# Performance work log

Hardware: AMD Instinct MI355X
Metric: run time of the kernel (lower is better)

The kernel has to match this reference:

```python
import jax, jax.numpy as jnp
import numpy as np

N_HEAD = 16
NEG = -1e9

def setup_inputs() -> dict:
    key = jax.random.key(0)
    k1, k2, k3 = jax.random.split(key, 3)
    B, S, NX = 8, 1024, 1024
    x = jax.random.normal(k1, (B, S, NX), dtype=jnp.float32)
    w_attn = jax.random.normal(k2, (NX, 3 * NX), dtype=jnp.float32) * 0.02
    b_attn = jnp.zeros((3 * NX,), dtype=jnp.float32)
    w_proj = jax.random.normal(k3, (NX, NX), dtype=jnp.float32) * 0.02
    b_proj = jnp.zeros((NX,), dtype=jnp.float32)
    return {"x": x, "w_attn": w_attn, "b_attn": b_attn, "w_proj": w_proj, "b_proj": b_proj}

def reference(x, w_attn, b_attn, w_proj, b_proj):
    B, S, NX = x.shape
    H = N_HEAD
    D = NX // H
    qkv = x @ w_attn + b_attn                      # [B,S,3*NX]
    q, k, v = jnp.split(qkv, 3, axis=-1)           # each [B,S,NX]
    q = q.reshape(B, S, H, D)
    k = k.reshape(B, S, H, D)
    v = v.reshape(B, S, H, D)
    # scores with scale (scale=True -> divide by sqrt(head_dim))
    w = jnp.einsum('bqhd,bkhd->bhqk', q, k) / jnp.sqrt(jnp.float32(D))
    tril = jnp.tril(jnp.ones((S, S), dtype=w.dtype))  # causal mask buffer
    w = w * tril + NEG * (1.0 - tril)
    w = jax.nn.softmax(w, axis=-1)                 # dropout is identity at eval
    a = jnp.einsum('bhqk,bkhd->bqhd', w, v)        # [B,S,H,D]
    a = a.reshape(B, S, NX)
    a = a @ w_proj + b_proj
    return a
```

## Files before the change

kernel.cpp:

```cpp
#include <hip/hip_runtime.h>
#include <hip/hip_bf16.h>
#include <stdint.h>

typedef __bf16 bf16x8 __attribute__((ext_vector_type(8)));
typedef float  f32x4  __attribute__((ext_vector_type(4)));
typedef float  f32x16 __attribute__((ext_vector_type(16)));

__device__ __forceinline__ void gload_lds16(const void* g, void* l) {
  __builtin_amdgcn_global_load_lds(
      (const __attribute__((address_space(1))) unsigned int*)g,
      (__attribute__((address_space(3))) unsigned int*)l, 16, 0, 0);
}

__global__ void k_cast(const float* __restrict__ in, __bf16* __restrict__ out, int n4) {
  int i = blockIdx.x * blockDim.x + threadIdx.x;
  if (i >= n4) return;
  float4 v = reinterpret_cast<const float4*>(in)[i];
  union { __bf16 h[4]; uint64_t u; } c;
  c.h[0] = (__bf16)v.x; c.h[1] = (__bf16)v.y; c.h[2] = (__bf16)v.z; c.h[3] = (__bf16)v.w;
  *reinterpret_cast<uint64_t*>(out + 4l * i) = c.u;
}

__global__ void k_transpose_cast(const float* __restrict__ in, __bf16* __restrict__ out,
                                 int R, int C) {
  __shared__ float t[32][33];
  const int tx = threadIdx.x & 31, ty = threadIdx.x >> 5;
  const int c0 = blockIdx.x * 32, r0 = blockIdx.y * 32;
#pragma unroll
  for (int rr = 0; rr < 4; ++rr)
    t[ty * 4 + rr][tx] = in[(long)(r0 + ty * 4 + rr) * C + c0 + tx];
  __syncthreads();
#pragma unroll
  for (int rr = 0; rr < 4; ++rr)
    out[(long)(c0 + ty * 4 + rr) * R + r0 + tx] = (__bf16)t[tx][ty * 4 + rr];
}

template <int MODE>
__global__ void k_gemm_bt(const __bf16* __restrict__ A, const __bf16* __restrict__ Bt,
                          const float* __restrict__ bias, int M, int N, int K,
                          __bf16* __restrict__ qo, __bf16* __restrict__ ko,
                          __bf16* __restrict__ vo, float* __restrict__ fo) {
  __shared__ __bf16 Ab[128 * 32];
  __shared__ __bf16 Bb[128 * 32];
  const int l = threadIdx.x & 63, w = threadIdx.x >> 6;
  const int wr = w >> 1, wc = w & 1;
  const int bm = blockIdx.y, bn = blockIdx.x;

  f32x4 acc[4][4] = {};

  const __bf16* Ag = A + (long)(bm * 128 + w * 32 + (l >> 2)) * K + (l & 3) * 8;
  const __bf16* Bg = Bt + (long)(bn * 128 + w * 32 + (l >> 2)) * K + (l & 3) * 8;
  char* Al = (char*)Ab + w * 2048;
  char* Bl = (char*)Bb + w * 2048;

  for (int k0 = 0; k0 < K; k0 += 32) {
    gload_lds16(Ag + k0, Al);
    gload_lds16(Ag + 16l * K + k0, Al + 1024);
    gload_lds16(Bg + k0, Bl);
    gload_lds16(Bg + 16l * K + k0, Bl + 1024);
    __syncthreads();

    bf16x8 af[4], bfr[4];
#pragma unroll
    for (int mi = 0; mi < 4; ++mi)
      af[mi] = *(const bf16x8*)&Ab[(wr * 64 + mi * 16 + (l & 15)) * 32 + ((l >> 4) << 3)];
#pragma unroll
    for (int ni = 0; ni < 4; ++ni)
      bfr[ni] = *(const bf16x8*)&Bb[(wc * 64 + ni * 16 + (l & 15)) * 32 + ((l >> 4) << 3)];
#pragma unroll
    for (int mi = 0; mi < 4; ++mi)
#pragma unroll
      for (int ni = 0; ni < 4; ++ni)
        acc[mi][ni] = __builtin_amdgcn_mfma_f32_16x16x32_bf16(af[mi], bfr[ni], acc[mi][ni], 0, 0, 0);
    __syncthreads();
  }

  if (MODE == 0) {
#pragma unroll
    for (int ni = 0; ni < 4; ++ni) {
      const int c = bn * 128 + wc * 64 + ni * 16 + (l & 15);
      const float bv = bias[c];
      const int which = c >> 10, cc = c & 1023, h = cc >> 6, d = cc & 63;
#pragma unroll
      for (int mi = 0; mi < 4; ++mi)
#pragma unroll
        for (int i = 0; i < 4; ++i) {
          const int r = bm * 128 + wr * 64 + mi * 16 + ((l >> 4) << 2) + i;
          const int b = r >> 10, s_ = r & 1023;
          float fv = acc[mi][ni][i] + bv;
          if (which == 0) fv *= 0.125f;
          const __bf16 v = (__bf16)fv;
          const long hb = (long)(b * 16 + h);
          if (which == 0)      qo[(hb * 1024 + s_) * 64 + d] = v;
          else if (which == 1) ko[(hb * 1024 + s_) * 64 + d] = v;
          else                 vo[(hb * 64 + d) * 1024 + s_] = v;
        }
    }
  } else {
#pragma unroll
    for (int ni = 0; ni < 4; ++ni) {
      const int c = bn * 128 + wc * 64 + ni * 16 + (l & 15);
      const float bv = bias[c];
#pragma unroll
      for (int mi = 0; mi < 4; ++mi)
#pragma unroll
        for (int i = 0; i < 4; ++i) {
          const int r = bm * 128 + wr * 64 + mi * 16 + ((l >> 4) << 2) + i;
          fo[(long)r * N + c] = acc[mi][ni][i] + bv;
        }
    }
  }
}

__device__ __forceinline__ void attn_qtile(const __bf16* __restrict__ Q,
                                           const __bf16* __restrict__ Kh,
                                           const __bf16* __restrict__ Vt,
                                           __bf16* __restrict__ ob,
                                           int b, int h, int qbw, int l) {
  const int lm = l & 31, hi = l >> 5;

  bf16x8 qf[4];
#pragma unroll
  for (int ds = 0; ds < 4; ++ds)
    qf[ds] = *(const bf16x8*)(Q + (long)(qbw + lm) * 64 + ds * 16 + hi * 8);

  f32x16 oacc0 = {}, oacc1 = {};
  float m = -__builtin_inff(), s = 0.f;

  const int ntiles = (qbw >> 5) + 1;
  for (int kt = 0; kt < ntiles; ++kt) {
    const int k0 = kt * 32;
    f32x16 st = {};
#pragma unroll
    for (int ds = 0; ds < 4; ++ds) {
      bf16x8 kf = *(const bf16x8*)(Kh + (long)(k0 + lm) * 64 + ds * 16 + hi * 8);
      st = __builtin_amdgcn_mfma_f32_32x32x16_bf16(kf, qf[ds], st, 0, 0, 0);
    }
    if (kt == ntiles - 1) {
      const int q = qbw + lm;
#pragma unroll
      for (int r = 0; r < 16; ++r) {
        const int key = k0 + (r & 3) + 8 * (r >> 2) + 4 * hi;
        if (key > q) st[r] = -__builtin_inff();
      }
    }
    float tm = st[0];
#pragma unroll
    for (int r = 1; r < 16; ++r) tm = fmaxf(tm, st[r]);
    tm = fmaxf(tm, __shfl_xor(tm, 32));
    if (!__all(tm <= m + 8.f)) {
      const float mn = fmaxf(m, tm);
      const float fac = __expf(m - mn);
      m = mn;
      s *= fac;
#pragma unroll
      for (int r = 0; r < 16; ++r) {
        const int qr = (r & 3) + 8 * (r >> 2) + 4 * hi;
        const float fr = __int_as_float(
            __builtin_amdgcn_ds_bpermute(qr * 4, __float_as_int(fac)));
        oacc0[r] *= fr; oacc1[r] *= fr;
      }
    }
    float p[16], ts = 0.f;
#pragma unroll
    for (int r = 0; r < 16; ++r) { p[r] = __expf(st[r] - m); ts += p[r]; }
    ts += __shfl_xor(ts, 32);
    s += ts;
    unsigned int w8[8];
#pragma unroll
    for (int t = 0; t < 8; ++t) {
      union { __bf16 hh[2]; unsigned int u; } pk;
      pk.hh[0] = (__bf16)p[2 * t]; pk.hh[1] = (__bf16)p[2 * t + 1];
      w8[t] = pk.u;
    }
    const unsigned int e0 = __shfl_xor(hi ? w8[0] : w8[2], 32);
    const unsigned int e1 = __shfl_xor(hi ? w8[1] : w8[3], 32);
    const unsigned int e2 = __shfl_xor(hi ? w8[4] : w8[6], 32);
    const unsigned int e3 = __shfl_xor(hi ? w8[5] : w8[7], 32);
    union { unsigned int wd[4]; bf16x8 v; } pa0, pa1;
    if (hi) {
      pa0.wd[0] = e0;    pa0.wd[1] = e1;    pa0.wd[2] = w8[2]; pa0.wd[3] = w8[3];
      pa1.wd[0] = e2;    pa1.wd[1] = e3;    pa1.wd[2] = w8[6]; pa1.wd[3] = w8[7];
    } else {
      pa0.wd[0] = w8[0]; pa0.wd[1] = w8[1]; pa0.wd[2] = e0;    pa0.wd[3] = e1;
      pa1.wd[0] = w8[4]; pa1.wd[1] = w8[5]; pa1.wd[2] = e2;    pa1.wd[3] = e3;
    }
#pragma unroll
    for (int t = 0; t < 2; ++t) {
      const bf16x8 pa = t ? pa1.v : pa0.v;
      bf16x8 vf0 = *(const bf16x8*)(Vt + (long)lm * 1024 + k0 + t * 16 + hi * 8);
      bf16x8 vf1 = *(const bf16x8*)(Vt + (long)(32 + lm) * 1024 + k0 + t * 16 + hi * 8);
      oacc0 = __builtin_amdgcn_mfma_f32_32x32x16_bf16(pa, vf0, oacc0, 0, 0, 0);
      oacc1 = __builtin_amdgcn_mfma_f32_32x32x16_bf16(pa, vf1, oacc1, 0, 0, 0);
    }
  }
  const float invs = 1.f / s;
#pragma unroll
  for (int r = 0; r < 16; ++r) {
    const int qr = (r & 3) + 8 * (r >> 2) + 4 * hi;
    const float inv = __int_as_float(
        __builtin_amdgcn_ds_bpermute(qr * 4, __float_as_int(invs)));
    const long row = (long)(b * 1024 + qbw + qr) * 1024 + h * 64;
    ob[row + lm]      = (__bf16)(oacc0[r] * inv);
    ob[row + 32 + lm] = (__bf16)(oacc1[r] * inv);
  }
}

__global__ void k_attn(const __bf16* __restrict__ qb_, const __bf16* __restrict__ kb,
                       const __bf16* __restrict__ vtb, __bf16* __restrict__ ob) {
  const int l = threadIdx.x & 63, w = threadIdx.x >> 6;
  const int bh = blockIdx.y, b = bh >> 4, h = bh & 15;
  const int wi = blockIdx.x * 4 + w;
  const __bf16* Q  = qb_ + (long)bh * 65536;
  const __bf16* Kh = kb  + (long)bh * 65536;
  const __bf16* Vt = vtb + (long)bh * 65536;
  attn_qtile(Q, Kh, Vt, ob, b, h, wi * 32, l);
  attn_qtile(Q, Kh, Vt, ob, b, h, (31 - wi) * 32, l);
}

extern "C" void kernel_launch(void* const* d_in, const int* in_sizes, int n_in,
                              void* d_out, int out_size, void* d_ws, size_t ws_size,
                              hipStream_t stream) {
  const float* x      = (const float*)d_in[0];
  const float* w_attn = (const float*)d_in[1];
  const float* b_attn = (const float*)d_in[2];
  const float* w_proj = (const float*)d_in[3];
  const float* b_proj = (const float*)d_in[4];
  float* out = (float*)d_out;

  char* ws = (char*)d_ws;
  const size_t SZ_XBF = (size_t)8192 * 1024 * 2;
  __bf16* x_bf = (__bf16*)ws;  ws += SZ_XBF;
  __bf16* wat  = (__bf16*)ws;  ws += (size_t)3072 * 1024 * 2;
  __bf16* wpt  = (__bf16*)ws;  ws += (size_t)1024 * 1024 * 2;
  __bf16* qb   = (__bf16*)ws;  ws += SZ_XBF;
  __bf16* kb   = (__bf16*)ws;  ws += SZ_XBF;
  __bf16* vtb  = (__bf16*)ws;  ws += SZ_XBF;
  __bf16* obf  = (__bf16*)ws;  ws += SZ_XBF;

  k_cast<<<8192, 256, 0, stream>>>(x, x_bf, 2097152);
  k_transpose_cast<<<dim3(96, 32), 256, 0, stream>>>(w_attn, wat, 1024, 3072);
  k_transpose_cast<<<dim3(32, 32), 256, 0, stream>>>(w_proj, wpt, 1024, 1024);
  k_gemm_bt<0><<<dim3(24, 64), 256, 0, stream>>>(x_bf, wat, b_attn, 8192, 3072, 1024,
                                                 qb, kb, vtb, nullptr);
  k_attn<<<dim3(4, 128), 256, 0, stream>>>(qb, kb, vtb, obf);
  k_gemm_bt<1><<<dim3(8, 64), 256, 0, stream>>>(obf, wpt, b_proj, 8192, 1024, 1024,
                                                nullptr, nullptr, nullptr, out);
}
```

Measured before the change: 286.9 us.

## Double-buffer swizzled GEMM, widen attention key tiles, add XCD-aware block mapping

The GEMM is rewritten with a 64-wide K step, a double-buffered LDS pipeline that uses explicit vmcnt waits, an XOR swizzle to avoid LDS bank conflicts, and MFMA priority boosting. Both GEMM and attention now map blocks so that neighbouring tiles or heads share an XCD for L2 reuse. The attention loop handles 64 keys per iteration instead of 32, which halves the number of softmax rescale and reduction steps. The trade-off is higher register pressure in attention and more LDS per block in the GEMM, which may lower occupancy.

```diff
diff --git a/kernel.cpp b/kernel.cpp
--- a/kernel.cpp
+++ b/kernel.cpp
@@ -5,6 +5,11 @@
 typedef __bf16 bf16x8 __attribute__((ext_vector_type(8)));
 typedef float  f32x4  __attribute__((ext_vector_type(4)));
 typedef float  f32x16 __attribute__((ext_vector_type(16)));
+
+#define BARRIER() asm volatile("s_barrier" ::: "memory")
+#define VMCNT(n)  asm volatile("s_waitcnt vmcnt(" #n ")" ::: "memory")
+#define LGKM0()   asm volatile("s_waitcnt lgkmcnt(0)" ::: "memory")
+#define SCHED0()  __builtin_amdgcn_sched_barrier(0)
 
 __device__ __forceinline__ void gload_lds16(const void* g, void* l) {
   __builtin_amdgcn_global_load_lds(
@@ -36,61 +41,98 @@
 }
 
 template <int MODE>
-__global__ void k_gemm_bt(const __bf16* __restrict__ A, const __bf16* __restrict__ Bt,
-                          const float* __restrict__ bias, int M, int N, int K,
-                          __bf16* __restrict__ qo, __bf16* __restrict__ ko,
-                          __bf16* __restrict__ vo, float* __restrict__ fo) {
-  __shared__ __bf16 Ab[128 * 32];
-  __shared__ __bf16 Bb[128 * 32];
-  const int l = threadIdx.x & 63, w = threadIdx.x >> 6;
-  const int wr = w >> 1, wc = w & 1;
-  const int bm = blockIdx.y, bn = blockIdx.x;
+__launch_bounds__(256, 2)
+__global__ void k_gemm2(const __bf16* __restrict__ A, const __bf16* __restrict__ Bt,
+                        const float* __restrict__ bias, int M, int N, int K, int NBX,
+                        __bf16* __restrict__ qo, __bf16* __restrict__ ko,
+                        __bf16* __restrict__ vo, float* __restrict__ fo) {
+  __shared__ __bf16 lds[2][2][8192];
+  const int tid = threadIdx.x;
+  const int l = tid & 63, w = tid >> 6;
+  const int lm = l & 15, lq = l >> 4;
+  const int wm = w >> 1, wn = w & 1;
+  const int xcd = blockIdx.x & 7, s = blockIdx.x >> 3;
+  const int bn = xcd * NBX + s % NBX;
+  const int bm = s / NBX;
+  const int nt = K >> 6;
+
+  const int rA = tid >> 3;
+  const int scol = (((tid & 7) * 16) ^ ((rA & 7) << 4)) >> 1;
+  long a_off[4], b_off[4];
+#pragma unroll
+  for (int li = 0; li < 4; ++li) {
+    a_off[li] = (long)(bm * 128 + li * 32 + rA) * K + scol;
+    b_off[li] = (long)(bn * 128 + li * 32 + rA) * K + scol;
+  }
+#define STAGE(buf, t) { \
+    gload_lds16(A + a_off[0] + (long)(t) * 64, &lds[buf][0][tid * 8]); \
+    gload_lds16(A + a_off[1] + (long)(t) * 64, &lds[buf][0][2048 + tid * 8]); \
+    gload_lds16(A + a_off[2] + (long)(t) * 64, &lds[buf][0][4096 + tid * 8]); \
+    gload_lds16(A + a_off[3] + (long)(t) * 64, &lds[buf][0][6144 + tid * 8]); \
+    gload_lds16(Bt + b_off[0] + (long)(t) * 64, &lds[buf][1][tid * 8]); \
+    gload_lds16(Bt + b_off[1] + (long)(t) * 64, &lds[buf][1][2048 + tid * 8]); \
+    gload_lds16(Bt + b_off[2] + (long)(t) * 64, &lds[buf][1][4096 + tid * 8]); \
+    gload_lds16(Bt + b_off[3] + (long)(t) * 64, &lds[buf][1][6144 + tid * 8]); }
+
+  const int aswz = (lm & 7) << 4;
+  const int cofs0 = ((0 * 64 + lq * 16) ^ aswz) >> 1;
+  const int cofs1 = ((1 * 64 + lq * 16) ^ aswz) >> 1;
+  const int arow = wm * 64 + lm;
+  const int brow = wn * 64 + lm;
 
   f32x4 acc[4][4] = {};
 
-  const __bf16* Ag = A + (long)(bm * 128 + w * 32 + (l >> 2)) * K + (l & 3) * 8;
-  const __bf16* Bg = Bt + (long)(bn * 128 + w * 32 + (l >> 2)) * K + (l & 3) * 8;
-  char* Al = (char*)Ab + w * 2048;
-  char* Bl = (char*)Bb + w * 2048;
-
-  for (int k0 = 0; k0 < K; k0 += 32) {
-    gload_lds16(Ag + k0, Al);
-    gload_lds16(Ag + 16l * K + k0, Al + 1024);
-    gload_lds16(Bg + k0, Bl);
-    gload_lds16(Bg + 16l * K + k0, Bl + 1024);
-    __syncthreads();
-
-    bf16x8 af[4], bfr[4];
-#pragma unroll
-    for (int mi = 0; mi < 4; ++mi)
-      af[mi] = *(const bf16x8*)&Ab[(wr * 64 + mi * 16 + (l & 15)) * 32 + ((l >> 4) << 3)];
-#pragma unroll
-    for (int ni = 0; ni < 4; ++ni)
-      bfr[ni] = *(const bf16x8*)&Bb[(wc * 64 + ni * 16 + (l & 15)) * 32 + ((l >> 4) << 3)];
-#pragma unroll
-    for (int mi = 0; mi < 4; ++mi)
-#pragma unroll
-      for (int ni = 0; ni < 4; ++ni)
-        acc[mi][ni] = __builtin_amdgcn_mfma_f32_16x16x32_bf16(af[mi], bfr[ni], acc[mi][ni], 0, 0, 0);
-    __syncthreads();
+  STAGE(0, 0);
+
+  for (int t = 0; t < nt; ++t) {
+    const int cur = t & 1;
+    if (t + 1 < nt) { STAGE(cur ^ 1, t + 1); VMCNT(8); }
+    else VMCNT(0);
+    BARRIER();
+    const __bf16* La = lds[cur][0];
+    const __bf16* Lbv = lds[cur][1];
+    bf16x8 af[4][2], bfr[4][2];
+#pragma unroll
+    for (int mi = 0; mi < 4; ++mi) {
+      af[mi][0] = *(const bf16x8*)&La[(arow + mi * 16) * 64 + cofs0];
+      af[mi][1] = *(const bf16x8*)&La[(arow + mi * 16) * 64 + cofs1];
+    }
+#pragma unroll
+    for (int ni = 0; ni < 4; ++ni) {
+      bfr[ni][0] = *(const bf16x8*)&Lbv[(brow + ni * 16) * 64 + cofs0];
+      bfr[ni][1] = *(const bf16x8*)&Lbv[(brow + ni * 16) * 64 + cofs1];
+    }
+    LGKM0(); SCHED0();
+    __builtin_amdgcn_s_setprio(1);
+#pragma unroll
+    for (int ks = 0; ks < 2; ++ks)
+#pragma unroll
+      for (int mi = 0; mi < 4; ++mi)
+#pragma unroll
+        for (int ni = 0; ni < 4; ++ni)
+          acc[mi][ni] = __builtin_amdgcn_mfma_f32_16x16x32_bf16(af[mi][ks], bfr[ni][ks],
+                                                                acc[mi][ni], 0, 0, 0);
+    __builtin_amdgcn_s_setprio(0);
+    SCHED0();
+    BARRIER();
   }
 
   if (MODE == 0) {
 #pragma unroll
     for (int ni = 0; ni < 4; ++ni) {
-      const int c = bn * 128 + wc * 64 + ni * 16 + (l & 15);
+      const int c = bn * 128 + wn * 64 + ni * 16 + lm;
       const float bv = bias[c];
-      const int which = c >> 10, cc = c & 1023, h = cc >> 6, d = cc & 63;
+      const int which = c >> 10, cc = c & 1023, hh = cc >> 6, d = cc & 63;
 #pragma unroll
       for (int mi = 0; mi < 4; ++mi)
 #pragma unroll
         for (int i = 0; i < 4; ++i) {
-          const int r = bm * 128 + wr * 64 + mi * 16 + ((l >> 4) << 2) + i;
+          const int r = bm * 128 + wm * 64 + mi * 16 + lq * 4 + i;
           const int b = r >> 10, s_ = r & 1023;
           float fv = acc[mi][ni][i] + bv;
           if (which == 0) fv *= 0.125f;
           const __bf16 v = (__bf16)fv;
-          const long hb = (long)(b * 16 + h);
+          const long hb = (long)(b * 16 + hh);
           if (which == 0)      qo[(hb * 1024 + s_) * 64 + d] = v;
           else if (which == 1) ko[(hb * 1024 + s_) * 64 + d] = v;
           else                 vo[(hb * 64 + d) * 1024 + s_] = v;
@@ -99,17 +141,18 @@
   } else {
 #pragma unroll
     for (int ni = 0; ni < 4; ++ni) {
-      const int c = bn * 128 + wc * 64 + ni * 16 + (l & 15);
+      const int c = bn * 128 + wn * 64 + ni * 16 + lm;
       const float bv = bias[c];
 #pragma unroll
       for (int mi = 0; mi < 4; ++mi)
 #pragma unroll
         for (int i = 0; i < 4; ++i) {
-          const int r = bm * 128 + wr * 64 + mi * 16 + ((l >> 4) << 2) + i;
+          const int r = bm * 128 + wm * 64 + mi * 16 + lq * 4 + i;
           fo[(long)r * N + c] = acc[mi][ni][i] + bv;
         }
     }
   }
+#undef STAGE
 }
 
 __device__ __forceinline__ void attn_qtile(const __bf16* __restrict__ Q,
@@ -127,26 +170,29 @@
   f32x16 oacc0 = {}, oacc1 = {};
   float m = -__builtin_inff(), s = 0.f;
 
-  const int ntiles = (qbw >> 5) + 1;
-  for (int kt = 0; kt < ntiles; ++kt) {
-    const int k0 = kt * 32;
-    f32x16 st = {};
+  const int nt64 = (qbw >> 6) + 1;
+  for (int kt = 0; kt < nt64; ++kt) {
+    const int k0 = kt * 64;
+    f32x16 st0 = {}, st1 = {};
 #pragma unroll
     for (int ds = 0; ds < 4; ++ds) {
-      bf16x8 kf = *(const bf16x8*)(Kh + (long)(k0 + lm) * 64 + ds * 16 + hi * 8);
-      st = __builtin_amdgcn_mfma_f32_32x32x16_bf16(kf, qf[ds], st, 0, 0, 0);
-    }
-    if (kt == ntiles - 1) {
+      bf16x8 kf0 = *(const bf16x8*)(Kh + (long)(k0 + lm) * 64 + ds * 16 + hi * 8);
+      bf16x8 kf1 = *(const bf16x8*)(Kh + (long)(k0 + 32 + lm) * 64 + ds * 16 + hi * 8);
+      st0 = __builtin_amdgcn_mfma_f32_32x32x16_bf16(kf0, qf[ds], st0, 0, 0, 0);
+      st1 = __builtin_amdgcn_mfma_f32_32x32x16_bf16(kf1, qf[ds], st1, 0, 0, 0);
+    }
+    if (kt == nt64 - 1) {
       const int q = qbw + lm;
 #pragma unroll
       for (int r = 0; r < 16; ++r) {
         const int key = k0 + (r & 3) + 8 * (r >> 2) + 4 * hi;
-        if (key > q) st[r] = -__builtin_inff();
+        if (key > q)      st0[r] = -__builtin_inff();
+        if (key + 32 > q) st1[r] = -__builtin_inff();
       }
     }
-    float tm = st[0];
-#pragma unroll
-    for (int r = 1; r < 16; ++r) tm = fmaxf(tm, st[r]);
+    float tm = fmaxf(st0[0], st1[0]);
+#pragma unroll
+    for (int r = 1; r < 16; ++r) tm = fmaxf(tm, fmaxf(st0[r], st1[r]));
     tm = fmaxf(tm, __shfl_xor(tm, 32));
     if (!__all(tm <= m + 8.f)) {
       const float mn = fmaxf(m, tm);
@@ -161,37 +207,59 @@
         oacc0[r] *= fr; oacc1[r] *= fr;
       }
     }
-    float p[16], ts = 0.f;
-#pragma unroll
-    for (int r = 0; r < 16; ++r) { p[r] = __expf(st[r] - m); ts += p[r]; }
+    float ts = 0.f;
+    unsigned int w8a[8], w8b[8];
+#pragma unroll
+    for (int t = 0; t < 8; ++t) {
+      const float pa_ = __expf(st0[2 * t] - m), pb_ = __expf(st0[2 * t + 1] - m);
+      ts += pa_ + pb_;
+      union { __bf16 hh[2]; unsigned int u; } pk;
+      pk.hh[0] = (__bf16)pa_; pk.hh[1] = (__bf16)pb_;
+      w8a[t] = pk.u;
+    }
+#pragma unroll
+    for (int t = 0; t < 8; ++t) {
+      const float pa_ = __expf(st1[2 * t] - m), pb_ = __expf(st1[2 * t + 1] - m);
+      ts += pa_ + pb_;
+      union { __bf16 hh[2]; unsigned int u; } pk;
+      pk.hh[0] = (__bf16)pa_; pk.hh[1] = (__bf16)pb_;
+      w8b[t] = pk.u;
+    }
     ts += __shfl_xor(ts, 32);
     s += ts;
-    unsigned int w8[8];
-#pragma unroll
-    for (int t = 0; t < 8; ++t) {
-      union { __bf16 hh[2]; unsigned int u; } pk;
-      pk.hh[0] = (__bf16)p[2 * t]; pk.hh[1] = (__bf16)p[2 * t + 1];
-      w8[t] = pk.u;
-    }
-    const unsigned int e0 = __shfl_xor(hi ? w8[0] : w8[2], 32);
-    const unsigned int e1 = __shfl_xor(hi ? w8[1] : w8[3], 32);
-    const unsigned int e2 = __shfl_xor(hi ? w8[4] : w8[6], 32);
-    const unsigned int e3 = __shfl_xor(hi ? w8[5] : w8[7], 32);
-    union { unsigned int wd[4]; bf16x8 v; } pa0, pa1;
-    if (hi) {
-      pa0.wd[0] = e0;    pa0.wd[1] = e1;    pa0.wd[2] = w8[2]; pa0.wd[3] = w8[3];
-      pa1.wd[0] = e2;    pa1.wd[1] = e3;    pa1.wd[2] = w8[6]; pa1.wd[3] = w8[7];
-    } else {
-      pa0.wd[0] = w8[0]; pa0.wd[1] = w8[1]; pa0.wd[2] = e0;    pa0.wd[3] = e1;
-      pa1.wd[0] = w8[4]; pa1.wd[1] = w8[5]; pa1.wd[2] = e2;    pa1.wd[3] = e3;
-    }
-#pragma unroll
-    for (int t = 0; t < 2; ++t) {
-      const bf16x8 pa = t ? pa1.v : pa0.v;
+    union { unsigned int wd[4]; bf16x8 v; } pa[4];
+    {
+      const unsigned int e0 = __shfl_xor(hi ? w8a[0] : w8a[2], 32);
+      const unsigned int e1 = __shfl_xor(hi ? w8a[1] : w8a[3], 32);
+      const unsigned int e2 = __shfl_xor(hi ? w8a[4] : w8a[6], 32);
+      const unsigned int e3 = __shfl_xor(hi ? w8a[5] : w8a[7], 32);
+      if (hi) {
+        pa[0].wd[0] = e0;     pa[0].wd[1] = e1;     pa[0].wd[2] = w8a[2]; pa[0].wd[3] = w8a[3];
+        pa[1].wd[0] = e2;     pa[1].wd[1] = e3;     pa[1].wd[2] = w8a[6]; pa[1].wd[3] = w8a[7];
+      } else {
+        pa[0].wd[0] = w8a[0]; pa[0].wd[1] = w8a[1]; pa[0].wd[2] = e0;     pa[0].wd[3] = e1;
+        pa[1].wd[0] = w8a[4]; pa[1].wd[1] = w8a[5]; pa[1].wd[2] = e2;     pa[1].wd[3] = e3;
+      }
+    }
+    {
+      const unsigned int e0 = __shfl_xor(hi ? w8b[0] : w8b[2], 32);
+      const unsigned int e1 = __shfl_xor(hi ? w8b[1] : w8b[3], 32);
+      const unsigned int e2 = __shfl_xor(hi ? w8b[4] : w8b[6], 32);
+      const unsigned int e3 = __shfl_xor(hi ? w8b[5] : w8b[7], 32);
+      if (hi) {
+        pa[2].wd[0] = e0;     pa[2].wd[1] = e1;     pa[2].wd[2] = w8b[2]; pa[2].wd[3] = w8b[3];
+        pa[3].wd[0] = e2;     pa[3].wd[1] = e3;     pa[3].wd[2] = w8b[6]; pa[3].wd[3] = w8b[7];
+      } else {
+        pa[2].wd[0] = w8b[0]; pa[2].wd[1] = w8b[1]; pa[2].wd[2] = e0;     pa[2].wd[3] = e1;
+        pa[3].wd[0] = w8b[4]; pa[3].wd[1] = w8b[5]; pa[3].wd[2] = e2;     pa[3].wd[3] = e3;
+      }
+    }
+#pragma unroll
+    for (int t = 0; t < 4; ++t) {
       bf16x8 vf0 = *(const bf16x8*)(Vt + (long)lm * 1024 + k0 + t * 16 + hi * 8);
       bf16x8 vf1 = *(const bf16x8*)(Vt + (long)(32 + lm) * 1024 + k0 + t * 16 + hi * 8);
-      oacc0 = __builtin_amdgcn_mfma_f32_32x32x16_bf16(pa, vf0, oacc0, 0, 0, 0);
-      oacc1 = __builtin_amdgcn_mfma_f32_32x32x16_bf16(pa, vf1, oacc1, 0, 0, 0);
+      oacc0 = __builtin_amdgcn_mfma_f32_32x32x16_bf16(pa[t].v, vf0, oacc0, 0, 0, 0);
+      oacc1 = __builtin_amdgcn_mfma_f32_32x32x16_bf16(pa[t].v, vf1, oacc1, 0, 0, 0);
     }
   }
   const float invs = 1.f / s;
@@ -209,8 +277,12 @@
 __global__ void k_attn(const __bf16* __restrict__ qb_, const __bf16* __restrict__ kb,
                        const __bf16* __restrict__ vtb, __bf16* __restrict__ ob) {
   const int l = threadIdx.x & 63, w = threadIdx.x >> 6;
-  const int bh = blockIdx.y, b = bh >> 4, h = bh & 15;
-  const int wi = blockIdx.x * 4 + w;
+  const int bid = blockIdx.x;
+  const int xcd = bid & 7, slot = bid >> 3;
+  const int bh = xcd + 8 * (slot >> 2);
+  const int j = slot & 3;
+  const int wi = j * 4 + w;
+  const int b = bh >> 4, h = bh & 15;
   const __bf16* Q  = qb_ + (long)bh * 65536;
   const __bf16* Kh = kb  + (long)bh * 65536;
   const __bf16* Vt = vtb + (long)bh * 65536;
@@ -241,9 +313,9 @@
   k_cast<<<8192, 256, 0, stream>>>(x, x_bf, 2097152);
   k_transpose_cast<<<dim3(96, 32), 256, 0, stream>>>(w_attn, wat, 1024, 3072);
   k_transpose_cast<<<dim3(32, 32), 256, 0, stream>>>(w_proj, wpt, 1024, 1024);
-  k_gemm_bt<0><<<dim3(24, 64), 256, 0, stream>>>(x_bf, wat, b_attn, 8192, 3072, 1024,
-                                                 qb, kb, vtb, nullptr);
-  k_attn<<<dim3(4, 128), 256, 0, stream>>>(qb, kb, vtb, obf);
-  k_gemm_bt<1><<<dim3(8, 64), 256, 0, stream>>>(obf, wpt, b_proj, 8192, 1024, 1024,
-                                                nullptr, nullptr, nullptr, out);
-}
+  k_gemm2<0><<<1536, 256, 0, stream>>>(x_bf, wat, b_attn, 8192, 3072, 1024, 3,
+                                       qb, kb, vtb, nullptr);
+  k_attn<<<512, 256, 0, stream>>>(qb, kb, vtb, obf);
+  k_gemm2<1><<<512, 256, 0, stream>>>(obf, wpt, b_proj, 8192, 1024, 1024, 1,
+                                      nullptr, nullptr, nullptr, out);
+}
```

Measured after the change: 285.9 us. About the same (-0.3%).
